# Performance work log

Hardware: AMD Instinct MI355X
Metric: run time of the kernel (lower is better)

The kernel has to match this reference:

```python
import jax, jax.numpy as jnp
import numpy as np

N = 50000   # nodes
E = 800000  # edges
F = 128     # input features
H = 128     # hidden channels
G = 64      # graphs in batch
C = 10      # classes
L_HID = 3   # residual hidden GCN blocks
EPS = 1e-5  # BatchNorm eps


def setup_inputs() -> dict:
    key = jax.random.key(0)
    ks = jax.random.split(key, 10)
    sc = lambda k, s: (jax.random.normal(k, s, jnp.float32) * 0.05)
    x = jax.random.normal(ks[0], (N, F), jnp.float32)
    edge_index = jax.random.randint(ks[1], (2, E), 0, N, dtype=jnp.int32)
    batch = jnp.sort(jax.random.randint(ks[2], (N,), 0, G, dtype=jnp.int32))
    return {
        "x": x, "edge_index": edge_index, "batch": batch,
        # initial GCN block
        "W0": sc(ks[3], (F, H)), "b0": jnp.zeros(H, jnp.float32),
        "g0": jnp.ones(H, jnp.float32), "be0": jnp.zeros(H, jnp.float32),
        # 3 residual GCN blocks (stacked)
        "Wh": sc(ks[4], (L_HID, H, H)), "bh": jnp.zeros((L_HID, H), jnp.float32),
        "gh": jnp.ones((L_HID, H), jnp.float32), "beh": jnp.zeros((L_HID, H), jnp.float32),
        "Rh": sc(ks[5], (L_HID, H, H)),  # residual Linear (no bias)
        # MLP head: Linear(H,H)+ReLU, Linear(H,C)
        "mW1": sc(ks[6], (H, H)), "mb1": jnp.zeros(H, jnp.float32),
        "mW2": sc(ks[7], (H, C)), "mb2": jnp.zeros(C, jnp.float32),
    }


def _gcn_norm(edge_index, n):
    # add self-loops + symmetric normalization, as in PyG GCNConv
    loop = jnp.arange(n, dtype=edge_index.dtype)
    src = jnp.concatenate([edge_index[0], loop])
    dst = jnp.concatenate([edge_index[1], loop])
    deg = jax.ops.segment_sum(jnp.ones_like(dst, jnp.float32), dst, num_segments=n)
    dinv = jnp.where(deg > 0, jax.lax.rsqrt(deg), 0.0)
    coef = dinv[src] * dinv[dst]  # [E+N]
    return src, dst, coef


def _gcn_conv(x, W, b, src, dst, coef, n):
    h = x @ W                                   # [N, H] linear first (PyG order)
    msg = h[src] * coef[:, None]                # gather + normalize  [E+N, H]
    agg = jax.ops.segment_sum(msg, dst, num_segments=n)  # scatter-add [N, H]
    return agg + b


def _bn_relu(h, gamma, beta):
    # BatchNorm1d in eval mode with running_mean=0, running_var=1
    inv = jax.lax.rsqrt(jnp.asarray(1.0 + EPS, h.dtype))
    return jax.nn.relu(h * inv * gamma + beta)  # dropout is identity in eval


def reference(x, edge_index, batch, W0, b0, g0, be0, Wh, bh, gh, beh, Rh, mW1, mb1, mW2, mb2):
    n = x.shape[0]
    src, dst, coef = _gcn_norm(edge_index, n)
    # initial block (no residual)
    h = _bn_relu(_gcn_conv(x, W0, b0, src, dst, coef, n), g0, be0)
    # residual hidden blocks
    for i in range(Wh.shape[0]):
        c = _gcn_conv(h, Wh[i], bh[i], src, dst, coef, n) + h @ Rh[i]
        h = _bn_relu(c, gh[i], beh[i])
    # global max pool over graphs in the batch
    pooled = jax.ops.segment_max(h, batch, num_segments=G)  # [G, H]
    # MLP head
    z = jax.nn.relu(pooled @ mW1 + mb1)
    return z @ mW2 + mb2  # [G, C]
```

## Files before the change

### kernel.cpp

```cpp
#include <hip/hip_runtime.h>
#include <cstdint>
#include <cstddef>

#define NN 50000
#define NE 800000
#define NEPAD (NE + 3 * NN)
#define HID 128
#define NGRAPH 64
#define NCLASS 10
#define LHID 3
#define NREP 8

#define ROWBLK 3125
#define ROWBLK_PAD 3128
#define GEMM_GRID 782
#define FILL_GRID 3125
#define FRONT_DEG 3125
#define FRONT_B 56
#define FRONT_GRID (FRONT_DEG + FRONT_B)

static constexpr float BN_INV = 0.9999950000374996f;

typedef __attribute__((ext_vector_type(8))) __bf16 bf16x8;
typedef __attribute__((ext_vector_type(4))) float floatx4;


__device__ __forceinline__ unsigned int f32_to_bf16_rne(float f) {
    unsigned int u = __float_as_uint(f);
    return (u + 0x7FFFu + ((u >> 16) & 1u)) >> 16;
}
__device__ __forceinline__ float bf16_to_f32(unsigned int h) {
    return __uint_as_float(h << 16);
}
__device__ __forceinline__ void split2(float a, float b, unsigned int& hi,
                                       unsigned int& lo) {
    unsigned int h0 = f32_to_bf16_rne(a), h1 = f32_to_bf16_rne(b);
    unsigned int l0 = f32_to_bf16_rne(a - bf16_to_f32(h0));
    unsigned int l1 = f32_to_bf16_rne(b - bf16_to_f32(h1));
    hi = h0 | (h1 << 16);
    lo = l0 | (l1 << 16);
}


__global__ void k_front(const float* __restrict__ W0, const float* __restrict__ Wh,
                        const float* __restrict__ Rh, unsigned short* __restrict__ bH,
                        unsigned short* __restrict__ bL,
                        const int* __restrict__ ei, int* __restrict__ deg8,
                        int* __restrict__ eslot) {
    const int b = blockIdx.x;
    const int tid = threadIdx.x;
    if (b < FRONT_DEG) {
        int e = b * 256 + tid;
        int d = ei[NE + e];
        int rep = e & (NREP - 1);
        eslot[e] = atomicAdd(&deg8[rep * NN + d], 1);
    } else {
        int cb = b - FRONT_DEG;
        int mat = cb >> 3;
        const float* src = (mat == 0) ? W0
                         : (mat <= 3) ? (Wh + (size_t)(mat - 1) * 16384)
                                      : (Rh + (size_t)(mat - 4) * 16384);
        int u = (cb & 7) * 256 + tid;
        int lane = u & 63;
        int blk = u >> 6;
        int kblk = blk & 3;
        int nb = blk >> 2;
        int n = nb * 16 + (lane & 15);
        int k = kblk * 32 + (lane >> 4) * 8;
        union { unsigned int i[4]; uint4 v; } H, L;
#pragma unroll
        for (int j = 0; j < 4; ++j) {
            float a = src[(size_t)(k + 2 * j) * 128 + n];
            float c = src[(size_t)(k + 2 * j + 1) * 128 + n];
            split2(a, c, H.i[j], L.i[j]);
        }
        size_t base = (size_t)mat * 16384 + (size_t)u * 8;
        *(uint4*)&bH[base] = H.v;
        *(uint4*)&bL[base] = L.v;
    }
}


__global__ void k_scan1(const int* __restrict__ deg8, int* __restrict__ degT,
                        int* __restrict__ degOff, float* __restrict__ dinv,
                        int* __restrict__ bsum) {
    __shared__ int s[256];
    int i = blockIdx.x * 256 + threadIdx.x;
    int dsum = 0;
    if (i < NN) {
        int off[NREP];
#pragma unroll
        for (int r = 0; r < NREP; ++r) {
            off[r] = dsum;
            dsum += deg8[r * NN + i];
        }
#pragma unroll
        for (int r = 0; r < NREP; ++r) degOff[i * NREP + r] = off[r];
        degT[i] = dsum;
        dinv[i] = rsqrtf((float)(dsum + 1));
    }
    s[threadIdx.x] = (dsum + 3) & ~3;
    __syncthreads();
    for (int o = 128; o > 0; o >>= 1) {
        if (threadIdx.x < o) s[threadIdx.x] += s[threadIdx.x + o];
        __syncthreads();
    }
    if (threadIdx.x == 0) bsum[blockIdx.x] = s[0];
}


__global__ void k_scan3(const int* __restrict__ degT, const int* __restrict__ bsum,
                        int* __restrict__ rowptr, int* __restrict__ col,
                        float* __restrict__ cfv) {
    __shared__ int s[256];
    __shared__ int offS;
    const int bid = blockIdx.x;
    s[threadIdx.x] = (threadIdx.x < bid) ? bsum[threadIdx.x] : 0;
    __syncthreads();
    for (int o = 128; o > 0; o >>= 1) {
        if (threadIdx.x < o) s[threadIdx.x] += s[threadIdx.x + o];
        __syncthreads();
    }
    if (threadIdx.x == 0) offS = s[0];
    __syncthreads();
    const int off = offS;
    __syncthreads();
    int i = bid * 256 + threadIdx.x;
    int d = (i < NN) ? degT[i] : 0;
    int v = (d + 3) & ~3;
    s[threadIdx.x] = v;
    __syncthreads();
    for (int o = 1; o < 256; o <<= 1) {
        int tv = (threadIdx.x >= o) ? s[threadIdx.x - o] : 0;
        __syncthreads();
        s[threadIdx.x] += tv;
        __syncthreads();
    }
    if (i < NN) {
        int rp = off + s[threadIdx.x] - v;
        rowptr[i] = rp;
        for (int p = rp + d; p < rp + v; ++p) { col[p] = 0; cfv[p] = 0.f; }
    }
}


template <int NB, bool FILL, bool XA>
__global__ __launch_bounds__(256, 3) void k_gemm_mfma(
    const float* __restrict__ X,
    const unsigned short* __restrict__ Ahi, const unsigned short* __restrict__ Alo,
    const unsigned short* __restrict__ B1hi, const unsigned short* __restrict__ B1lo,
    const unsigned short* __restrict__ B2hi, const unsigned short* __restrict__ B2lo,
    float* __restrict__ C1, float* __restrict__ C2,
    const int* __restrict__ ei, const int* __restrict__ rowptr,
    const int* __restrict__ eslot, const int* __restrict__ degOff,
    const float* __restrict__ dinv, int* __restrict__ col,
    float* __restrict__ cfv) {
    if (FILL && blockIdx.x >= GEMM_GRID) {
        int e = (blockIdx.x - GEMM_GRID) * 256 + threadIdx.x;
        int s = ei[e];
        int d = ei[NE + e];
        int rep = e & (NREP - 1);
        int p = rowptr[d] + degOff[d * NREP + rep] + eslot[e];
        col[p] = s;
        cfv[p] = dinv[s];
        return;
    }
    const int tid = threadIdx.x;
    const int wave = tid >> 6;
    const int lane = tid & 63;
    const int wm = wave & 1;
    const int wn = wave >> 1;
    const int rb0 = blockIdx.x * 4;

    floatx4 acc1[2][4], acc2[2][4];
    floatx4 zero = {0.f, 0.f, 0.f, 0.f};
#pragma unroll
    for (int i = 0; i < 2; ++i)
#pragma unroll
        for (int j = 0; j < 4; ++j) { acc1[i][j] = zero; if (NB == 2) acc2[i][j] = zero; }

#pragma unroll
    for (int kc = 0; kc < 4; ++kc) {
        bf16x8 aH[2], aL[2], bH[4], bL[4];
        if (XA) {
#pragma unroll
            for (int t = 0; t < 2; ++t) {
                int m = (rb0 + wm * 2 + t) * 16 + (lane & 15);
                if (m >= NN) m = NN - 1;
                const float4* p =
                    (const float4*)&X[(size_t)m * 128 + kc * 32 + (lane >> 4) * 8];
                float4 v0 = p[0];
                float4 v1 = p[1];
                float vals[8] = {v0.x, v0.y, v0.z, v0.w, v1.x, v1.y, v1.z, v1.w};
                union { unsigned int i[4]; bf16x8 v; } H, L;
#pragma unroll
                for (int j = 0; j < 4; ++j)
                    split2(vals[2 * j], vals[2 * j + 1], H.i[j], L.i[j]);
                aH[t] = H.v;
                aL[t] = L.v;
            }
        } else {
#pragma unroll
            for (int t = 0; t < 2; ++t) {
                size_t u = ((size_t)(rb0 + wm * 2 + t) * 4 + kc) * 512 + lane * 8;
                aH[t] = *(const bf16x8*)(Ahi + u);
                aL[t] = *(const bf16x8*)(Alo + u);
            }
        }
#pragma unroll
        for (int t = 0; t < 4; ++t)
            bH[t] = *(const bf16x8*)(B1hi + ((size_t)(wn * 4 + t) * 4 + kc) * 512 +
                                     lane * 8);
#pragma unroll
        for (int tm = 0; tm < 2; ++tm)
#pragma unroll
            for (int tn = 0; tn < 4; ++tn)
                acc1[tm][tn] = __builtin_amdgcn_mfma_f32_16x16x32_bf16(
                    aH[tm], bH[tn], acc1[tm][tn], 0, 0, 0);
#pragma unroll
        for (int t = 0; t < 4; ++t)
            bL[t] = *(const bf16x8*)(B1lo + ((size_t)(wn * 4 + t) * 4 + kc) * 512 +
                                     lane * 8);
#pragma unroll
        for (int tm = 0; tm < 2; ++tm)
#pragma unroll
            for (int tn = 0; tn < 4; ++tn)
                acc1[tm][tn] = __builtin_amdgcn_mfma_f32_16x16x32_bf16(
                    aH[tm], bL[tn], acc1[tm][tn], 0, 0, 0);
#pragma unroll
        for (int tm = 0; tm < 2; ++tm)
#pragma unroll
            for (int tn = 0; tn < 4; ++tn)
                acc1[tm][tn] = __builtin_amdgcn_mfma_f32_16x16x32_bf16(
                    aL[tm], bH[tn], acc1[tm][tn], 0, 0, 0);
        if (NB == 2) {
#pragma unroll
            for (int t = 0; t < 4; ++t)
                bH[t] = *(const bf16x8*)(B2hi + ((size_t)(wn * 4 + t) * 4 + kc) * 512 +
                                         lane * 8);
#pragma unroll
            for (int tm = 0; tm < 2; ++tm)
#pragma unroll
                for (int tn = 0; tn < 4; ++tn)
                    acc2[tm][tn] = __builtin_amdgcn_mfma_f32_16x16x32_bf16(
                        aH[tm], bH[tn], acc2[tm][tn], 0, 0, 0);
#pragma unroll
            for (int tm = 0; tm < 2; ++tm)
#pragma unroll
                for (int tn = 0; tn < 4; ++tn)
                    acc2[tm][tn] = __builtin_amdgcn_mfma_f32_16x16x32_bf16(
                        aL[tm], bH[tn], acc2[tm][tn], 0, 0, 0);
#pragma unroll
            for (int t = 0; t < 4; ++t)
                bL[t] = *(const bf16x8*)(B2lo + ((size_t)(wn * 4 + t) * 4 + kc) * 512 +
                                         lane * 8);
#pragma unroll
            for (int tm = 0; tm < 2; ++tm)
#pragma unroll
                for (int tn = 0; tn < 4; ++tn)
                    acc2[tm][tn] = __builtin_amdgcn_mfma_f32_16x16x32_bf16(
                        aH[tm], bL[tn], acc2[tm][tn], 0, 0, 0);
        }
    }

    const int quad = lane >> 4;
    const int col0 = lane & 15;
    const int rowBase = blockIdx.x * 64 + wm * 32;
#pragma unroll
    for (int tm = 0; tm < 2; ++tm) {
#pragma unroll
        for (int tn = 0; tn < 4; ++tn) {
            int c = wn * 64 + tn * 16 + col0;
#pragma unroll
            for (int r = 0; r < 4; ++r) {
                int row = rowBase + tm * 16 + quad * 4 + r;
                if (row < NN) {
                    C1[(size_t)row * 128 + c] = acc1[tm][tn][r];
                    if (NB == 2) C2[(size_t)row * 128 + c] = acc2[tm][tn][r];
                }
            }
        }
    }
}


template <bool RES, bool LAST>
__global__ __launch_bounds__(1024, 8) void k_spmm(
    const float* __restrict__ t, const float* __restrict__ r,
    const int* __restrict__ rowptr, const int* __restrict__ degT,
    const int* __restrict__ col, const float* __restrict__ cfv,
    const float* __restrict__ dinv, const float* __restrict__ bias,
    const float* __restrict__ gamma, const float* __restrict__ beta,
    const unsigned short* __restrict__ w1H, const unsigned short* __restrict__ w1L,
    const unsigned short* __restrict__ w2H, const unsigned short* __restrict__ w2L,
    float* __restrict__ tOut, float* __restrict__ rOut,
    const int* __restrict__ batch, float* __restrict__ pooled) {
    __shared__ unsigned short shU[2][16][16][8];
    __shared__ float shP[16][128];
    const int tid = threadIdx.x;
    const int lane = tid & 63;
    const int h = lane >> 5;
    const int f4 = lane & 31;
    const int wv = __builtin_amdgcn_readfirstlane(tid >> 6);
    const int node = blockIdx.x * 16 + wv;

    const int start = __builtin_amdgcn_readfirstlane(rowptr[node]);
    const int cnt4 = __builtin_amdgcn_readfirstlane((degT[node] + 3) >> 2);

    float4 acc = {0.f, 0.f, 0.f, 0.f};
#pragma unroll 4
    for (int q = 0; q < cnt4; ++q) {
        const int4 cs = *(const int4*)(col + start + q * 4);
        const float4 wvv = *(const float4*)(cfv + start + q * 4);
        const int rowA = h ? cs.y : cs.x;
        const int rowB = h ? cs.w : cs.z;
        const float wA = h ? wvv.y : wvv.x;
        const float wB = h ? wvv.w : wvv.z;
        const float4 vA = *(const float4*)&t[(size_t)rowA * 128 + f4 * 4];
        const float4 vB = *(const float4*)&t[(size_t)rowB * 128 + f4 * 4];
        acc.x = fmaf(wA, vA.x, acc.x); acc.y = fmaf(wA, vA.y, acc.y);
        acc.z = fmaf(wA, vA.z, acc.z); acc.w = fmaf(wA, vA.w, acc.w);
        acc.x = fmaf(wB, vB.x, acc.x); acc.y = fmaf(wB, vB.y, acc.y);
        acc.z = fmaf(wB, vB.z, acc.z); acc.w = fmaf(wB, vB.w, acc.w);
    }
    acc.x += __shfl_xor(acc.x, 32);
    acc.y += __shfl_xor(acc.y, 32);
    acc.z += __shfl_xor(acc.z, 32);
    acc.w += __shfl_xor(acc.w, 32);

    const int f0 = f4 * 4;
    float4 o;
    if (h == 0) {
        const float di = dinv[node];
        const float dii = di * di;
        const float4 tv = *(const float4*)&t[(size_t)node * 128 + f0];
        const float4 bv = *(const float4*)&bias[f0];
        const float4 gv = *(const float4*)&gamma[f0];
        const float4 ev = *(const float4*)&beta[f0];
        float4 cc;
        cc.x = di * acc.x + dii * tv.x + bv.x;
        cc.y = di * acc.y + dii * tv.y + bv.y;
        cc.z = di * acc.z + dii * tv.z + bv.z;
        cc.w = di * acc.w + dii * tv.w + bv.w;
        if (RES) {
            const float4 rv = *(const float4*)&r[(size_t)node * 128 + f0];
            cc.x += rv.x; cc.y += rv.y; cc.z += rv.z; cc.w += rv.w;
        }
        o.x = fmaxf(cc.x * (BN_INV * gv.x) + ev.x, 0.f);
        o.y = fmaxf(cc.y * (BN_INV * gv.y) + ev.y, 0.f);
        o.z = fmaxf(cc.z * (BN_INV * gv.z) + ev.z, 0.f);
        o.w = fmaxf(cc.w * (BN_INV * gv.w) + ev.w, 0.f);
    }

    if (LAST) {
        bool uni = (batch[blockIdx.x * 16] == batch[blockIdx.x * 16 + 15]);
        if (uni) {
            if (h == 0) *(float4*)&shP[wv][f0] = o;
            __syncthreads();
            if (wv == 0) {
                float a = shP[0][2 * lane], b = shP[0][2 * lane + 1];
#pragma unroll
                for (int w = 1; w < 16; ++w) {
                    a = fmaxf(a, shP[w][2 * lane]);
                    b = fmaxf(b, shP[w][2 * lane + 1]);
                }
                int g = batch[blockIdx.x * 16];
                atomicMax((unsigned int*)&pooled[g * 128 + 2 * lane],
                          __float_as_uint(a));
                atomicMax((unsigned int*)&pooled[g * 128 + 2 * lane + 1],
                          __float_as_uint(b));
            }
        } else if (h == 0) {
            int g = batch[node];
            atomicMax((unsigned int*)&pooled[g * 128 + f0], __float_as_uint(o.x));
            atomicMax((unsigned int*)&pooled[g * 128 + f0 + 1], __float_as_uint(o.y));
            atomicMax((unsigned int*)&pooled[g * 128 + f0 + 2], __float_as_uint(o.z));
            atomicMax((unsigned int*)&pooled[g * 128 + f0 + 3], __float_as_uint(o.w));
        }
        return;
    }

    if (h == 0) {
        unsigned int H0, L0, H1, L1;
        split2(o.x, o.y, H0, L0);
        split2(o.z, o.w, H1, L1);
        const int u = f4 >> 1;
        const int ro = wv ^ u;
        const int so = (f4 & 1) * 4;
        uint2 Hv; Hv.x = H0; Hv.y = H1;
        uint2 Lv; Lv.x = L0; Lv.y = L1;
        *(uint2*)&shU[0][u][ro][so] = Hv;
        *(uint2*)&shU[1][u][ro][so] = Lv;
    }

    const int w = tid >> 6;
    const int mat = w >> 3;
    const int nb = w & 7;
    const unsigned short* BH = mat ? w2H : w1H;
    const unsigned short* BL = mat ? w2L : w1L;
    bf16x8 bHr[4], bLr[4];
#pragma unroll
    for (int kc = 0; kc < 4; ++kc) {
        bHr[kc] = *(const bf16x8*)(BH + ((size_t)nb * 4 + kc) * 512 + lane * 8);
        bLr[kc] = *(const bf16x8*)(BL + ((size_t)nb * 4 + kc) * 512 + lane * 8);
    }
    __syncthreads();

    float* outp = mat ? rOut : tOut;
    floatx4 accG = {0.f, 0.f, 0.f, 0.f};
#pragma unroll
    for (int kc = 0; kc < 4; ++kc) {
        const int uu = kc * 4 + (lane >> 4);
        const int rr = (lane & 15) ^ uu;
        bf16x8 aH = *(const bf16x8*)&shU[0][uu][rr][0];
        bf16x8 aL = *(const bf16x8*)&shU[1][uu][rr][0];
        accG = __builtin_amdgcn_mfma_f32_16x16x32_bf16(aH, bHr[kc], accG, 0, 0, 0);
        accG = __builtin_amdgcn_mfma_f32_16x16x32_bf16(aH, bLr[kc], accG, 0, 0, 0);
        accG = __builtin_amdgcn_mfma_f32_16x16x32_bf16(aL, bHr[kc], accG, 0, 0, 0);
    }
    const int quad = lane >> 4;
    const int c0 = nb * 16 + (lane & 15);
    const int row0 = blockIdx.x * 16 + quad * 4;
#pragma unroll
    for (int rr2 = 0; rr2 < 4; ++rr2)
        outp[(size_t)(row0 + rr2) * 128 + c0] = accG[rr2];
}


__global__ void k_head(const float* __restrict__ pooled, const float* __restrict__ mW1,
                       const float* __restrict__ mb1, const float* __restrict__ mW2,
                       const float* __restrict__ mb2, float* __restrict__ out) {
    __shared__ float p[128];
    __shared__ float z[128];
    int g = blockIdx.x;
    int j = threadIdx.x;
    p[j] = pooled[g * 128 + j];
    __syncthreads();
    float a = mb1[j];
#pragma unroll 8
    for (int k = 0; k < 128; ++k) a += p[k] * mW1[k * 128 + j];
    z[j] = fmaxf(a, 0.f);
    __syncthreads();
    if (j < NCLASS) {
        float o = mb2[j];
#pragma unroll 8
        for (int k = 0; k < 128; ++k) o += z[k] * mW2[k * NCLASS + j];
        out[g * NCLASS + j] = o;
    }
}


extern "C" void kernel_launch(void* const* d_in, const int* in_sizes, int n_in,
                              void* d_out, int out_size, void* d_ws, size_t ws_size,
                              hipStream_t stream) {
    const float* x   = (const float*)d_in[0];
    const int*   ei  = (const int*)d_in[1];
    const int* batch = (const int*)d_in[2];
    const float* W0  = (const float*)d_in[3];
    const float* b0  = (const float*)d_in[4];
    const float* g0  = (const float*)d_in[5];
    const float* be0 = (const float*)d_in[6];
    const float* Wh  = (const float*)d_in[7];
    const float* bh  = (const float*)d_in[8];
    const float* gh  = (const float*)d_in[9];
    const float* beh = (const float*)d_in[10];
    const float* Rh  = (const float*)d_in[11];
    const float* mW1 = (const float*)d_in[12];
    const float* mb1 = (const float*)d_in[13];
    const float* mW2 = (const float*)d_in[14];
    const float* mb2 = (const float*)d_in[15];
    float* out = (float*)d_out;

    char* ws = (char*)d_ws;
    size_t off = 0;
    auto alloc = [&](size_t bytes) -> void* {
        void* p = ws + off;
        off += (bytes + 255) & ~(size_t)255;
        return p;
    };
    int*   deg8   = (int*)alloc((size_t)NREP * NN * 4);
    float* pooled = (float*)alloc((size_t)NGRAPH * HID * 4);
    size_t zspan = (size_t)((char*)pooled - (char*)deg8) + (size_t)NGRAPH * HID * 4;
    int*   degT   = (int*)alloc((size_t)NN * 4);
    int*   degOff = (int*)alloc((size_t)NN * NREP * 4);
    int*   rowptr = (int*)alloc((size_t)NN * 4);
    float* dinv   = (float*)alloc((size_t)NN * 4);
    int*   bsum   = (int*)alloc(256 * 4);
    int*   eslot  = (int*)alloc((size_t)NE * 4);
    int*   col    = (int*)alloc((size_t)NEPAD * 4);
    float* cfv    = (float*)alloc((size_t)NEPAD * 4);
    float* tA     = (float*)alloc((size_t)NN * HID * 4);
    float* tB     = (float*)alloc((size_t)NN * HID * 4);
    float* rA     = (float*)alloc((size_t)NN * HID * 4);
    float* rB     = (float*)alloc((size_t)NN * HID * 4);
    unsigned short* bH = (unsigned short*)alloc((size_t)7 * 16384 * 2);
    unsigned short* bL = (unsigned short*)alloc((size_t)7 * 16384 * 2);

    hipMemsetAsync(deg8, 0, zspan, stream);

    k_front<<<FRONT_GRID, 256, 0, stream>>>(W0, Wh, Rh, bH, bL, ei, deg8, eslot);
    k_scan1<<<(NN + 255) / 256, 256, 0, stream>>>(deg8, degT, degOff, dinv, bsum);
    k_scan3<<<(NN + 255) / 256, 256, 0, stream>>>(degT, bsum, rowptr, col, cfv);

    k_gemm_mfma<1, true, true><<<GEMM_GRID + FILL_GRID, 256, 0, stream>>>(
        x, nullptr, nullptr, bH, bL, nullptr, nullptr, tA, nullptr,
        ei, rowptr, eslot, degOff, dinv, col, cfv);

    const int spmmGrid = NN / 16;

    k_spmm<false, false><<<spmmGrid, 1024, 0, stream>>>(
        tA, nullptr, rowptr, degT, col, cfv, dinv, b0, g0, be0,
        bH + (size_t)1 * 16384, bL + (size_t)1 * 16384,
        bH + (size_t)4 * 16384, bL + (size_t)4 * 16384,
        tB, rB, nullptr, nullptr);

    k_spmm<true, false><<<spmmGrid, 1024, 0, stream>>>(
        tB, rB, rowptr, degT, col, cfv, dinv, bh + 0 * HID, gh + 0 * HID,
        beh + 0 * HID,
        bH + (size_t)2 * 16384, bL + (size_t)2 * 16384,
        bH + (size_t)5 * 16384, bL + (size_t)5 * 16384,
        tA, rA, nullptr, nullptr);

    k_spmm<true, false><<<spmmGrid, 1024, 0, stream>>>(
        tA, rA, rowptr, degT, col, cfv, dinv, bh + 1 * HID, gh + 1 * HID,
        beh + 1 * HID,
        bH + (size_t)3 * 16384, bL + (size_t)3 * 16384,
        bH + (size_t)6 * 16384, bL + (size_t)6 * 16384,
        tB, rB, nullptr, nullptr);

    k_spmm<true, true><<<spmmGrid, 1024, 0, stream>>>(
        tB, rB, rowptr, degT, col, cfv, dinv, bh + 2 * HID, gh + 2 * HID,
        beh + 2 * HID,
        nullptr, nullptr, nullptr, nullptr,
        nullptr, nullptr, batch, pooled);

    k_head<<<NGRAPH, 128, 0, stream>>>(pooled, mW1, mb1, mW2, mb2, out);
}
```

Measured before the change: 444.0 us.

## Pack CSR column and degree into one meta word; fill CSR with atomic cursors

The separate col and cfv arrays become one 32-bit meta word per edge. The low 17 bits hold the source node and the upper bits hold the source degree, and the SpMM rebuilds the normalisation weight with rsqrt on the fly. Padding slots are marked with the sign bit so their weight is zero. The CSR fill now takes slots from a per-row atomic cursor instead of precomputed eslot and degOff arrays, and degree counting reads four destinations per thread. This halves per-edge metadata traffic in every SpMM layer and removes preprocessing buffers. In exchange it adds an rsqrt per edge, and the edge order within a row, and so the float summation order, is no longer deterministic.

Result: no change. 451.6 us (+1.7%).

```diff
diff --git a/kernel.cpp b/kernel.cpp
--- a/kernel.cpp
+++ b/kernel.cpp
@@ -15,7 +15,7 @@
 #define ROWBLK_PAD 3128
 #define GEMM_GRID 782
 #define FILL_GRID 3125
-#define FRONT_DEG 3125
+#define FRONT_DEG 782
 #define FRONT_B 56
 #define FRONT_GRID (FRONT_DEG + FRONT_B)
 
@@ -45,15 +45,19 @@
 __global__ void k_front(const float* __restrict__ W0, const float* __restrict__ Wh,
                         const float* __restrict__ Rh, unsigned short* __restrict__ bH,
                         unsigned short* __restrict__ bL,
-                        const int* __restrict__ ei, int* __restrict__ deg8,
-                        int* __restrict__ eslot) {
+                        const int* __restrict__ ei, int* __restrict__ deg8) {
     const int b = blockIdx.x;
     const int tid = threadIdx.x;
     if (b < FRONT_DEG) {
-        int e = b * 256 + tid;
-        int d = ei[NE + e];
-        int rep = e & (NREP - 1);
-        eslot[e] = atomicAdd(&deg8[rep * NN + d], 1);
+        int e4 = b * 256 + tid;
+        if (e4 < NE / 4) {
+            const int4 d4 = *(const int4*)&ei[NE + e4 * 4];
+            const int r0 = (e4 * 4) & (NREP - 1);
+            atomicAdd(&deg8[((r0 + 0) & (NREP - 1)) * NN + d4.x], 1);
+            atomicAdd(&deg8[((r0 + 1) & (NREP - 1)) * NN + d4.y], 1);
+            atomicAdd(&deg8[((r0 + 2) & (NREP - 1)) * NN + d4.z], 1);
+            atomicAdd(&deg8[((r0 + 3) & (NREP - 1)) * NN + d4.w], 1);
+        }
     } else {
         int cb = b - FRONT_DEG;
         int mat = cb >> 3;
@@ -82,22 +86,17 @@
 
 
 __global__ void k_scan1(const int* __restrict__ deg8, int* __restrict__ degT,
-                        int* __restrict__ degOff, float* __restrict__ dinv,
+                        float* __restrict__ dinv, int* __restrict__ cur,
                         int* __restrict__ bsum) {
     __shared__ int s[256];
     int i = blockIdx.x * 256 + threadIdx.x;
     int dsum = 0;
     if (i < NN) {
-        int off[NREP];
-#pragma unroll
-        for (int r = 0; r < NREP; ++r) {
-            off[r] = dsum;
-            dsum += deg8[r * NN + i];
-        }
-#pragma unroll
-        for (int r = 0; r < NREP; ++r) degOff[i * NREP + r] = off[r];
+#pragma unroll
+        for (int r = 0; r < NREP; ++r) dsum += deg8[r * NN + i];
         degT[i] = dsum;
         dinv[i] = rsqrtf((float)(dsum + 1));
+        cur[i] = 0;
     }
     s[threadIdx.x] = (dsum + 3) & ~3;
     __syncthreads();
@@ -110,8 +109,7 @@
 
 
 __global__ void k_scan3(const int* __restrict__ degT, const int* __restrict__ bsum,
-                        int* __restrict__ rowptr, int* __restrict__ col,
-                        float* __restrict__ cfv) {
+                        int* __restrict__ rowptr, int* __restrict__ meta) {
     __shared__ int s[256];
     __shared__ int offS;
     const int bid = blockIdx.x;
@@ -139,7 +137,7 @@
     if (i < NN) {
         int rp = off + s[threadIdx.x] - v;
         rowptr[i] = rp;
-        for (int p = rp + d; p < rp + v; ++p) { col[p] = 0; cfv[p] = 0.f; }
+        for (int p = rp + d; p < rp + v; ++p) meta[p] = (int)0x80000000u;
     }
 }
 
@@ -152,17 +150,14 @@
     const unsigned short* __restrict__ B2hi, const unsigned short* __restrict__ B2lo,
     float* __restrict__ C1, float* __restrict__ C2,
     const int* __restrict__ ei, const int* __restrict__ rowptr,
-    const int* __restrict__ eslot, const int* __restrict__ degOff,
-    const float* __restrict__ dinv, int* __restrict__ col,
-    float* __restrict__ cfv) {
+    const int* __restrict__ degT, int* __restrict__ cur,
+    int* __restrict__ meta) {
     if (FILL && blockIdx.x >= GEMM_GRID) {
         int e = (blockIdx.x - GEMM_GRID) * 256 + threadIdx.x;
         int s = ei[e];
         int d = ei[NE + e];
-        int rep = e & (NREP - 1);
-        int p = rowptr[d] + degOff[d * NREP + rep] + eslot[e];
-        col[p] = s;
-        cfv[p] = dinv[s];
+        int slot = atomicAdd(&cur[d], 1);
+        meta[rowptr[d] + slot] = s | (degT[s] << 17);
         return;
     }
     const int tid = threadIdx.x;
@@ -288,9 +283,9 @@
 __global__ __launch_bounds__(1024, 8) void k_spmm(
     const float* __restrict__ t, const float* __restrict__ r,
     const int* __restrict__ rowptr, const int* __restrict__ degT,
-    const int* __restrict__ col, const float* __restrict__ cfv,
-    const float* __restrict__ dinv, const float* __restrict__ bias,
-    const float* __restrict__ gamma, const float* __restrict__ beta,
+    const int* __restrict__ meta, const float* __restrict__ dinv,
+    const float* __restrict__ bias, const float* __restrict__ gamma,
+    const float* __restrict__ beta,
     const unsigned short* __restrict__ w1H, const unsigned short* __restrict__ w1L,
     const unsigned short* __restrict__ w2H, const unsigned short* __restrict__ w2L,
     float* __restrict__ tOut, float* __restrict__ rOut,
@@ -310,12 +305,15 @@
     float4 acc = {0.f, 0.f, 0.f, 0.f};
 #pragma unroll 4
     for (int q = 0; q < cnt4; ++q) {
-        const int4 cs = *(const int4*)(col + start + q * 4);
-        const float4 wvv = *(const float4*)(cfv + start + q * 4);
-        const int rowA = h ? cs.y : cs.x;
-        const int rowB = h ? cs.w : cs.z;
-        const float wA = h ? wvv.y : wvv.x;
-        const float wB = h ? wvv.w : wvv.z;
+        const int4 m4 = *(const int4*)(meta + start + q * 4);
+        const unsigned int mvA = (unsigned int)(h ? m4.y : m4.x);
+        const unsigned int mvB = (unsigned int)(h ? m4.w : m4.z);
+        const int rowA = (int)(mvA & 0x1FFFFu);
+        const int rowB = (int)(mvB & 0x1FFFFu);
+        float wA = rsqrtf((float)((mvA >> 17) + 1u));
+        float wB = rsqrtf((float)((mvB >> 17) + 1u));
+        wA = ((int)mvA < 0) ? 0.f : wA;
+        wB = ((int)mvB < 0) ? 0.f : wB;
         const float4 vA = *(const float4*)&t[(size_t)rowA * 128 + f4 * 4];
         const float4 vB = *(const float4*)&t[(size_t)rowB * 128 + f4 * 4];
         acc.x = fmaf(wA, vA.x, acc.x); acc.y = fmaf(wA, vA.y, acc.y);
@@ -482,13 +480,11 @@
     float* pooled = (float*)alloc((size_t)NGRAPH * HID * 4);
     size_t zspan = (size_t)((char*)pooled - (char*)deg8) + (size_t)NGRAPH * HID * 4;
     int*   degT   = (int*)alloc((size_t)NN * 4);
-    int*   degOff = (int*)alloc((size_t)NN * NREP * 4);
     int*   rowptr = (int*)alloc((size_t)NN * 4);
     float* dinv   = (float*)alloc((size_t)NN * 4);
+    int*   cur    = (int*)alloc((size_t)NN * 4);
     int*   bsum   = (int*)alloc(256 * 4);
-    int*   eslot  = (int*)alloc((size_t)NE * 4);
-    int*   col    = (int*)alloc((size_t)NEPAD * 4);
-    float* cfv    = (float*)alloc((size_t)NEPAD * 4);
+    int*   meta   = (int*)alloc((size_t)NEPAD * 4);
     float* tA     = (float*)alloc((size_t)NN * HID * 4);
     float* tB     = (float*)alloc((size_t)NN * HID * 4);
     float* rA     = (float*)alloc((size_t)NN * HID * 4);
@@ -498,38 +494,38 @@
 
     hipMemsetAsync(deg8, 0, zspan, stream);
 
-    k_front<<<FRONT_GRID, 256, 0, stream>>>(W0, Wh, Rh, bH, bL, ei, deg8, eslot);
-    k_scan1<<<(NN + 255) / 256, 256, 0, stream>>>(deg8, degT, degOff, dinv, bsum);
-    k_scan3<<<(NN + 255) / 256, 256, 0, stream>>>(degT, bsum, rowptr, col, cfv);
+    k_front<<<FRONT_GRID, 256, 0, stream>>>(W0, Wh, Rh, bH, bL, ei, deg8);
+    k_scan1<<<(NN + 255) / 256, 256, 0, stream>>>(deg8, degT, dinv, cur, bsum);
+    k_scan3<<<(NN + 255) / 256, 256, 0, stream>>>(degT, bsum, rowptr, meta);
 
     k_gemm_mfma<1, true, true><<<GEMM_GRID + FILL_GRID, 256, 0, stream>>>(
         x, nullptr, nullptr, bH, bL, nullptr, nullptr, tA, nullptr,
-        ei, rowptr, eslot, degOff, dinv, col, cfv);
+        ei, rowptr, degT, cur, meta);
 
     const int spmmGrid = NN / 16;
 
     k_spmm<false, false><<<spmmGrid, 1024, 0, stream>>>(
-        tA, nullptr, rowptr, degT, col, cfv, dinv, b0, g0, be0,
+        tA, nullptr, rowptr, degT, meta, dinv, b0, g0, be0,
         bH + (size_t)1 * 16384, bL + (size_t)1 * 16384,
         bH + (size_t)4 * 16384, bL + (size_t)4 * 16384,
         tB, rB, nullptr, nullptr);
 
     k_spmm<true, false><<<spmmGrid, 1024, 0, stream>>>(
-        tB, rB, rowptr, degT, col, cfv, dinv, bh + 0 * HID, gh + 0 * HID,
+        tB, rB, rowptr, degT, meta, dinv, bh + 0 * HID, gh + 0 * HID,
         beh + 0 * HID,
         bH + (size_t)2 * 16384, bL + (size_t)2 * 16384,
         bH + (size_t)5 * 16384, bL + (size_t)5 * 16384,
         tA, rA, nullptr, nullptr);
 
     k_spmm<true, false><<<spmmGrid, 1024, 0, stream>>>(
-        tA, rA, rowptr, degT, col, cfv, dinv, bh + 1 * HID, gh + 1 * HID,
+        tA, rA, rowptr, degT, meta, dinv, bh + 1 * HID, gh + 1 * HID,
         beh + 1 * HID,
         bH + (size_t)3 * 16384, bL + (size_t)3 * 16384,
         bH + (size_t)6 * 16384, bL + (size_t)6 * 16384,
         tB, rB, nullptr, nullptr);
 
     k_spmm<true, true><<<spmmGrid, 1024, 0, stream>>>(
-        tB, rB, rowptr, degT, col, cfv, dinv, bh + 2 * HID, gh + 2 * HID,
+        tB, rB, rowptr, degT, meta, dinv, bh + 2 * HID, gh + 2 * HID,
         beh + 2 * HID,
         nullptr, nullptr, nullptr, nullptr,
         nullptr, nullptr, batch, pooled);
```
